# Optimization experiments

Hardware: AMD Instinct MI355X
Metric: run time of the kernel (lower is better)

## Reference

```python
import jax, jax.numpy as jnp
import numpy as np

K = 20        # kNN neighborhood size (args.k)
EPS = 1e-5    # BatchNorm eps
SLOPE = 0.2   # LeakyReLU negative slope
B, N = 8, 2048


def lrelu(x):
    return jnp.where(x >= 0, x, SLOPE * x)


def bn_cn(x):  # BatchNorm1d over [B, C, N] (training-mode batch stats, gamma=1, beta=0)
    m = jnp.mean(x, axis=(0, 2), keepdims=True)
    v = jnp.var(x, axis=(0, 2), keepdims=True)
    return (x - m) * jax.lax.rsqrt(v + EPS)


def bn_f(x):  # BatchNorm1d over [B, F]
    m = jnp.mean(x, axis=0, keepdims=True)
    v = jnp.var(x, axis=0, keepdims=True)
    return (x - m) * jax.lax.rsqrt(v + EPS)


def conv_bn(x, w):  # 1x1 Conv1d (no bias) + BN + LeakyReLU; x [B,C,N], w [O,C]
    return lrelu(bn_cn(jnp.einsum('oc,bcn->bon', w, x)))


def knn_idx(x, k):  # x [B,C,N] -> [B,N,k] nearest neighbors, self excluded
    sq = jnp.sum(x * x, axis=1)                                   # [B,N]
    pd = 2.0 * jnp.einsum('bcn,bcm->bnm', x, x) - sq[:, :, None] - sq[:, None, :]
    return jax.lax.top_k(pd, k + 1)[1][:, :, 1:]                  # drop self (max = 0)


def self_att(x, wq, wk, wv, wc):  # SelfAttention block (n_heads=1, scale_dot)
    idx = knn_idx(x, K)                                           # [B,N,K]
    feats = jnp.swapaxes(x, 1, 2)                                 # [B,N,C]
    nb = jax.vmap(lambda f, i: f[i])(feats, idx)                  # [B,N,K,C] gather
    E = wq.shape[0]
    q = feats @ wq.T                                              # [B,N,E]
    kk = nb @ wk.T                                                # [B,N,K,E]
    v = (nb - feats[:, :, None, :]) @ wv.T                        # [B,N,K,V]
    scores = jax.nn.softmax(jnp.einsum('bne,bnke->bnk', q, kk) / np.float32(np.sqrt(E)), axis=-1)
    out = jnp.einsum('bnk,bnkv->bnv', scores, v)                  # [B,N,V]
    res = conv_bn(jnp.swapaxes(out, 1, 2), wc)                    # [B,O,N]
    return jnp.concatenate([res, x], axis=1)


def setup_inputs() -> dict:
    key = jax.random.key(0)
    ks = jax.random.split(key, 32)
    w = lambda k, o, i: jax.random.normal(k, (o, i), jnp.float32) / np.float32(np.sqrt(i))
    d = {'x': jax.random.normal(ks[0], (B, 3, N), jnp.float32)}
    dims = {1: 3, 2: 64, 3: 64, 4: 128}
    j = 1
    for s, c in dims.items():
        for nm in ('wq', 'wk', 'wv', 'wc'):
            d[f'sa{s}_{nm}'] = w(ks[j], c, c); j += 1
    d['conv1_w'] = w(ks[17], 64, 6)
    d['conv2_w'] = w(ks[18], 64, 128)
    d['conv3_w'] = w(ks[19], 128, 128)
    d['conv4_w'] = w(ks[20], 256, 256)
    d['conv5_w'] = w(ks[21], 1024, 512)
    d['lin1_w'] = w(ks[22], 512, 2048); d['lin1_b'] = jnp.zeros((512,), jnp.float32)
    d['lin2_w'] = w(ks[23], 256, 512);  d['lin2_b'] = jnp.zeros((256,), jnp.float32)
    d['lin3_w'] = w(ks[24], 40, 256);   d['lin3_b'] = jnp.zeros((40,), jnp.float32)
    return d


def reference(x, sa1_wq, sa1_wk, sa1_wv, sa1_wc, sa2_wq, sa2_wk, sa2_wv, sa2_wc,
              sa3_wq, sa3_wk, sa3_wv, sa3_wc, sa4_wq, sa4_wk, sa4_wv, sa4_wc,
              conv1_w, conv2_w, conv3_w, conv4_w, conv5_w,
              lin1_w, lin1_b, lin2_w, lin2_b, lin3_w, lin3_b):
    h = self_att(x, sa1_wq, sa1_wk, sa1_wv, sa1_wc)        # [B,6,N]
    x1 = conv_bn(h, conv1_w)                               # [B,64,N]
    h = self_att(x1, sa2_wq, sa2_wk, sa2_wv, sa2_wc)       # [B,128,N]
    x2 = conv_bn(h, conv2_w)                               # [B,64,N]
    h = self_att(x2, sa3_wq, sa3_wk, sa3_wv, sa3_wc)       # [B,128,N]
    x3 = conv_bn(h, conv3_w)                               # [B,128,N]
    h = self_att(x3, sa4_wq, sa4_wk, sa4_wv, sa4_wc)       # [B,256,N]
    x4 = conv_bn(h, conv4_w)                               # [B,256,N]
    xc = jnp.concatenate([x1, x2, x3, x4], axis=1)         # [B,512,N]
    x5 = conv_bn(xc, conv5_w)                              # [B,1024,N]
    p = jnp.concatenate([jnp.max(x5, axis=2), jnp.mean(x5, axis=2)], axis=1)  # [B,2048]
    h = lrelu(bn_f(p @ lin1_w.T + lin1_b))                 # dropout = identity (eval)
    h = lrelu(bn_f(h @ lin2_w.T + lin2_b))
    return h @ lin3_w.T + lin3_b                           # [B,40]
```

## Files before the change

kernel.cpp:

```cpp
#include <hip/hip_runtime.h>
#include <math.h>

#define BB 8
#define NN 2048
#define KNB 20

typedef __attribute__((ext_vector_type(8))) short bf16x8;
typedef __attribute__((ext_vector_type(8))) _Float16 f16x8;
typedef __attribute__((ext_vector_type(4))) float f32x4;

__device__ inline unsigned short f2bf(float f) {
  union { float f; unsigned u; } v; v.f = f;
  unsigned r = v.u + 0x7FFF + ((v.u >> 16) & 1);
  return (unsigned short)(r >> 16);
}

__device__ inline float lrelu(float v) { return v >= 0.f ? v : 0.2f * v; }

template <bool F16SPLIT, bool BF16>
__global__ __launch_bounds__(256) void xprep_kernel(
    const float* __restrict__ in, int inBS, int C,
    float* __restrict__ xT, _Float16* __restrict__ hi, _Float16* __restrict__ lo,
    unsigned short* __restrict__ bf, float* __restrict__ sq) {
  __shared__ float tile[32][33];
// ... 5 lines not shown
  int tx = threadIdx.x & 31, ty = threadIdx.x >> 5;
  float s = 0.f;
  for (int yy = ty; yy < 32; yy += 8) {
    int r = r0 + yy;
    float v = (r < C) ? ip[(size_t)r * NN + c0 + tx] : 0.f;
    tile[yy][tx] = v;
    s += v * v;
  }
  ps[ty][tx] = s;
  __syncthreads();
  if (ty == 0) {
    float a = ps[0][tx];
#pragma unroll
    for (int u = 1; u < 8; ++u) a += ps[u][tx];
    atomicAdd(&sq[b * NN + c0 + tx], a);
  }
  for (int yy = ty; yy < 32; yy += 8) {
    int c = c0 + yy, r = r0 + tx;
    if (r < C) {
      float v = tile[tx][yy];
      size_t o = (size_t)b * NN * C + (size_t)c * C + r;
      xT[o] = v;
      if (F16SPLIT) {
        _Float16 hv = (_Float16)v;
        hi[o] = hv;
        lo[o] = (_Float16)(v - (float)hv);
      }
      if (BF16) bf[o] = f2bf(v);
    }
  }
}

__global__ __launch_bounds__(256) void xprep3_kernel(const float* __restrict__ in,
                                                     float* __restrict__ xT,
                                                     float* __restrict__ xs4) {
  int b = blockIdx.z;
  int n = blockIdx.x * 256 + threadIdx.x;
  const float* ip = in + (size_t)b * 3 * NN;
  float x0 = ip[n], x1 = ip[NN + n], x2 = ip[2 * NN + n];
  float s = x0 * x0 + x1 * x1 + x2 * x2;
  size_t o = (size_t)b * NN + n;
  xT[o * 3 + 0] = x0; xT[o * 3 + 1] = x1; xT[o * 3 + 2] = x2;
  *(float4*)&xs4[o * 4] = make_float4(x0, x1, x2, s);
}

__device__ inline void mw_task(const float* __restrict__ wq, const float* __restrict__ wk,
                               const float* __restrict__ wv, const float* __restrict__ wc,
                               int C, float* __restrict__ M, float* __restrict__ WCV,
                               unsigned short* __restrict__ Mb, unsigned short* __restrict__ wcvb,
                               bool emitBF, int w, int lane) {
  int total = 2 * C * C;
  if (w >= total) return;
  float a = 0.f;
  if (w < C * C) {
    int c = w / C, cp = w - c * C;
    for (int e = lane; e < C; e += 64) a += wk[e * C + c] * wq[e * C + cp];
  } else {
    int t = w - C * C;
    int o = t / C, c = t - o * C;
    for (int e = lane; e < C; e += 64) a += wc[o * C + e] * wv[e * C + c];
  }
#pragma unroll
  for (int s = 32; s > 0; s >>= 1) a += __shfl_down(a, s);
  if (lane == 0) {
    if (w < C * C) {
      M[w] = a;
      if (emitBF) Mb[w] = f2bf(a);
    } else {
      int t = w - C * C;
      WCV[t] = a;
      if (emitBF) wcvb[t] = f2bf(a);
    }
  }
}

// ... 11 lines not shown
  int wv_ = threadIdx.x >> 6;
  if (bx < 5) {
    mw_task(wq1, wk1, wv1, wc1, 3, M1, W1, nullptr, nullptr, false, bx * 4 + wv_, lane);
    return;
  }
  bx -= 5;
  if (bx < 2048) {
    mw_task(wq2, wk2, wv2, wc2, 64, M2, W2, nullptr, nullptr, false, bx * 4 + wv_, lane);
    return;
  }
  bx -= 2048;
  if (bx < 2048) {
    mw_task(wq3, wk3, wv3, wc3, 64, M3, W3, nullptr, nullptr, false, bx * 4 + wv_, lane);
    return;
  }
  bx -= 2048;
  if (bx < 8192) {
    mw_task(wq4, wk4, wv4, wc4, 128, M4, W4, Mb4, wcvb4, true, bx * 4 + wv_, lane);
    return;
  }
  bx -= 8192;
  if (bx < 256) {
    int i = bx * 256 + threadIdx.x;
    w4b[i] = f2bf(conv4_w[i]);
    return;
  }
  bx -= 256;
  {
    int i = bx * 256 + threadIdx.x;
    w5b[i] = f2bf(conv5_w[i]);
  }
}

__global__ __launch_bounds__(256) void transpose_kernel(const float* __restrict__ in, int inBS,
                                                        int R, int Cl, float* __restrict__ out) {
  __shared__ float tile[32][33];
  int b = blockIdx.z;
  const float* ip = in + (size_t)b * inBS;
  float* op = out + (size_t)b * R * Cl;
  int c0 = blockIdx.x * 32, r0 = blockIdx.y * 32;
  int tx = threadIdx.x & 31, ty = threadIdx.x >> 5;
  for (int yy = ty; yy < 32; yy += 8) {
    int r = r0 + yy, c = c0 + tx;
    tile[yy][tx] = (r < R && c < Cl) ? ip[(size_t)r * Cl + c] : 0.f;
  }
  __syncthreads();
  for (int yy = ty; yy < 32; yy += 8) {
    int c = c0 + yy, r = r0 + tx;
    if (c < Cl && r < R) op[(size_t)c * R + r] = tile[tx][yy];
  }
}

__global__ __launch_bounds__(256) void transpose_bf16_kernel(const float* __restrict__ in, int inBS,
                                                             int R, int Cl,
                                                             unsigned short* __restrict__ out) {
  __shared__ float tile[32][33];
  int b = blockIdx.z;
  const float* ip = in + (size_t)b * inBS;
  unsigned short* op = out + (size_t)b * R * Cl;
  int c0 = blockIdx.x * 32, r0 = blockIdx.y * 32;
  int tx = threadIdx.x & 31, ty = threadIdx.x >> 5;
  for (int yy = ty; yy < 32; yy += 8) {
    int r = r0 + yy, c = c0 + tx;
    tile[yy][tx] = (r < R && c < Cl) ? ip[(size_t)r * Cl + c] : 0.f;
  }
  __syncthreads();
  for (int yy = ty; yy < 32; yy += 8) {
    int c = c0 + yy, r = r0 + tx;
    if (c < Cl && r < R) op[(size_t)c * R + r] = f2bf(tile[tx][yy]);
  }
}

template <bool TOUT, bool STATS>
__global__ __launch_bounds__(256, 2) void mfma_gemm_lds_kernel(
    const unsigned short* __restrict__ A, const unsigned short* __restrict__ B,
    float* __restrict__ Z, int O, int K, float* __restrict__ gstats) {
  const int b = blockIdx.z;
  const int n0 = blockIdx.x * 128, o0 = blockIdx.y * 128;
  const int tid = threadIdx.x;
  const int wave = tid >> 6, lane = tid & 63;
  const int wo = wave >> 1, wn = wave & 1;
  const int l16 = lane & 15, q = lane >> 4;
  __shared__ unsigned short Al[2][4096];
  __shared__ unsigned short Bl[2][4096];
  const unsigned short* Ab = A + (size_t)o0 * K;
  const unsigned short* Bb = B + ((size_t)b * NN + n0) * K;

  const int p0 = tid, p1 = tid + 256;
  const int r0 = ((p0 >> 6) << 4) | (p0 & 15), c0 = ((p0 >> 4) & 3) * 8;
  const int r1 = ((p1 >> 6) << 4) | (p1 & 15), c1 = ((p1 >> 4) & 3) * 8;

  bf16x8 ar0, ar1, br0, br1;
  auto gload = [&](int k0) {
    ar0 = *(const bf16x8*)(Ab + (size_t)r0 * K + k0 + c0);
    ar1 = *(const bf16x8*)(Ab + (size_t)r1 * K + k0 + c1);
    br0 = *(const bf16x8*)(Bb + (size_t)r0 * K + k0 + c0);
    br1 = *(const bf16x8*)(Bb + (size_t)r1 * K + k0 + c1);
  };
  auto sstore = [&](int buf) {
    *(bf16x8*)&Al[buf][p0 * 8] = ar0;
    *(bf16x8*)&Al[buf][p1 * 8] = ar1;
    *(bf16x8*)&Bl[buf][p0 * 8] = br0;
    *(bf16x8*)&Bl[buf][p1 * 8] = br1;
  };

  f32x4 acc[4][4];
#pragma unroll
  for (int s = 0; s < 4; ++s)
#pragma unroll
    for (int t = 0; t < 4; ++t) acc[s][t] = (f32x4){0.f, 0.f, 0.f, 0.f};

  gload(0);
  sstore(0);
  int cur = 0;
  for (int k0 = 0; k0 < K; k0 += 32) {
    bool more = (k0 + 32) < K;
    if (more) gload(k0 + 32);
    __syncthreads();
    bf16x8 af[4], bfr[4];
#pragma unroll
    for (int s = 0; s < 4; ++s)
      af[s] = *(const bf16x8*)&Al[cur][((wo * 4 + s) * 64 + q * 16 + l16) * 8];
#pragma unroll
    for (int t = 0; t < 4; ++t)
      bfr[t] = *(const bf16x8*)&Bl[cur][((wn * 4 + t) * 64 + q * 16 + l16) * 8];
#pragma unroll
    for (int s = 0; s < 4; ++s)
#pragma unroll
      for (int t = 0; t < 4; ++t)
        acc[s][t] = __builtin_amdgcn_mfma_f32_16x16x32_bf16(af[s], bfr[t], acc[s][t], 0, 0, 0);
    if (more) sstore(cur ^ 1);
    cur ^= 1;
  }
#pragma unroll
  for (int s = 0; s < 4; ++s)
#pragma unroll
    for (int t = 0; t < 4; ++t) {
      if (TOUT) {
        int n = n0 + wn * 64 + t * 16 + l16;
        int ob = o0 + wo * 64 + s * 16 + q * 4;
        *(f32x4*)&Z[((size_t)b * NN + n) * O + ob] = acc[s][t];
      } else {
        float* zp = Z + ((size_t)b * O + o0 + wo * 64 + s * 16 + q * 4) * NN
                    + n0 + wn * 64 + t * 16 + l16;
#pragma unroll
        for (int r = 0; r < 4; ++r) zp[(size_t)r * NN] = acc[s][t][r];
      }
    }
  if (STATS) {
    float psum[16], psq[16];
#pragma unroll
    for (int s = 0; s < 4; ++s)
#pragma unroll
      for (int r = 0; r < 4; ++r) {
        float a = 0.f, sa = 0.f;
#pragma unroll
        for (int t = 0; t < 4; ++t) { float v = acc[s][t][r]; a += v; sa += v * v; }
        psum[s * 4 + r] = a; psq[s * 4 + r] = sa;
      }
#pragma unroll
    for (int i = 0; i < 16; ++i) {
#pragma unroll
      for (int mm = 1; mm < 16; mm <<= 1) {
        psum[i] += __shfl_xor(psum[i], mm);
        psq[i] += __shfl_xor(psq[i], mm);
      }
    }
    __syncthreads();
    float* sb = (float*)&Al[0][0];
    sb[tid] = 0.f;
    __syncthreads();
    if (l16 == 0) {
#pragma unroll
      for (int i = 0; i < 16; ++i) {
        int ch = wo * 64 + (i >> 2) * 16 + q * 4 + (i & 3);
        atomicAdd(&sb[ch * 2], psum[i]);
        atomicAdd(&sb[ch * 2 + 1], psq[i]);
      }
    }
    __syncthreads();
    atomicAdd(&gstats[o0 * 2 + tid], sb[tid]);
  }
}

__global__ __launch_bounds__(256, 2) void pd_mfma_sym_kernel(
    const _Float16* __restrict__ xhi, const _Float16* __restrict__ xlo, int C,
    const float* __restrict__ sq, float* __restrict__ P, int b_base) {
  const int bl = blockIdx.y;
  const int b = b_base + bl;
  int ti = 0, xx = blockIdx.x;
  while (xx >= 16 - ti) { xx -= 16 - ti; ++ti; }
  const int tj = ti + xx;
  const int n0 = ti * 128, m0 = tj * 128;
  const int tid = threadIdx.x;
  const int wave = tid >> 6, lane = tid & 63;
  const int wn_ = wave >> 1, wm_ = wave & 1;
  const int l16 = lane & 15, q = lane >> 4;
  __shared__ _Float16 Ah[4096], Al[4096], Bh[4096], Bl[4096];
  const _Float16* Ahg = xhi + ((size_t)b * NN + n0) * C;
  const _Float16* Alg = xlo + ((size_t)b * NN + n0) * C;
  const _Float16* Bhg = xhi + ((size_t)b * NN + m0) * C;
  const _Float16* Blg = xlo + ((size_t)b * NN + m0) * C;

  const int p0 = tid, p1 = tid + 256;
  const int r0 = ((p0 >> 6) << 4) | (p0 & 15), c0 = ((p0 >> 4) & 3) * 8;
  const int r1 = ((p1 >> 6) << 4) | (p1 & 15), c1 = ((p1 >> 4) & 3) * 8;

  f32x4 acc[4][4];
#pragma unroll
  for (int s = 0; s < 4; ++s)
#pragma unroll
    for (int t = 0; t < 4; ++t) acc[s][t] = (f32x4){0.f, 0.f, 0.f, 0.f};

  for (int k0 = 0; k0 < C; k0 += 32) {
    __syncthreads();
    *(f16x8*)&Ah[p0 * 8] = *(const f16x8*)(Ahg + (size_t)r0 * C + k0 + c0);
    *(f16x8*)&Ah[p1 * 8] = *(const f16x8*)(Ahg + (size_t)r1 * C + k0 + c1);
    *(f16x8*)&Al[p0 * 8] = *(const f16x8*)(Alg + (size_t)r0 * C + k0 + c0);
    *(f16x8*)&Al[p1 * 8] = *(const f16x8*)(Alg + (size_t)r1 * C + k0 + c1);
    *(f16x8*)&Bh[p0 * 8] = *(const f16x8*)(Bhg + (size_t)r0 * C + k0 + c0);
    *(f16x8*)&Bh[p1 * 8] = *(const f16x8*)(Bhg + (size_t)r1 * C + k0 + c1);
    *(f16x8*)&Bl[p0 * 8] = *(const f16x8*)(Blg + (size_t)r0 * C + k0 + c0);
    *(f16x8*)&Bl[p1 * 8] = *(const f16x8*)(Blg + (size_t)r1 * C + k0 + c1);
    __syncthreads();
    f16x8 ah[4], al[4], bh[4], blv[4];
#pragma unroll
    for (int s = 0; s < 4; ++s) {
      int pi = ((wn_ * 4 + s) * 64 + q * 16 + l16) * 8;
      ah[s] = *(const f16x8*)&Ah[pi];
      al[s] = *(const f16x8*)&Al[pi];
    }
#pragma unroll
    for (int t = 0; t < 4; ++t) {
      int pi = ((wm_ * 4 + t) * 64 + q * 16 + l16) * 8;
      bh[t] = *(const f16x8*)&Bh[pi];
      blv[t] = *(const f16x8*)&Bl[pi];
    }
#pragma unroll
    for (int s = 0; s < 4; ++s)
#pragma unroll
      for (int t = 0; t < 4; ++t) {
        acc[s][t] = __builtin_amdgcn_mfma_f32_16x16x32_f16(ah[s], bh[t], acc[s][t], 0, 0, 0);
        acc[s][t] = __builtin_amdgcn_mfma_f32_16x16x32_f16(ah[s], blv[t], acc[s][t], 0, 0, 0);
        acc[s][t] = __builtin_amdgcn_mfma_f32_16x16x32_f16(al[s], bh[t], acc[s][t], 0, 0, 0);
      }
  }
#pragma unroll
  for (int s = 0; s < 4; ++s)
#pragma unroll
    for (int t = 0; t < 4; ++t) {
      int col = m0 + wm_ * 64 + t * 16 + l16;
      float sqv = sq[b * NN + col];
      float* pp = P + ((size_t)bl * NN + n0 + wn_ * 64 + s * 16 + q * 4) * NN + col;
#pragma unroll
      for (int r = 0; r < 4; ++r) pp[(size_t)r * NN] = 2.f * acc[s][t][r] - sqv;
    }
  if (ti != tj) {
#pragma unroll
    for (int s = 0; s < 4; ++s) {
      int nb = n0 + wn_ * 64 + s * 16 + q * 4;
      float4 sqn = *(const float4*)&sq[b * NN + nb];
#pragma unroll
      for (int t = 0; t < 4; ++t) {
        int m = m0 + wm_ * 64 + t * 16 + l16;
        f32x4 ov;
        ov[0] = 2.f * acc[s][t][0] - sqn.x;
        ov[1] = 2.f * acc[s][t][1] - sqn.y;
        ov[2] = 2.f * acc[s][t][2] - sqn.z;
        ov[3] = 2.f * acc[s][t][3] - sqn.w;
        *(f32x4*)&P[((size_t)bl * NN + m) * NN + nb] = ov;
      }
    }
  }
}

__global__ __launch_bounds__(256) void topk_bsort_kernel(const float* __restrict__ P,
                                                         int* __restrict__ idx_out, int b_base) {
  const int wave = threadIdx.x >> 6;
// ... 75 lines not shown
#pragma unroll
    for (int j = k >> 1; j > 0; j >>= 1) {
#pragma unroll
      for (int i = 0; i < 32; ++i) {
        int l = i ^ j;
        if (l > i) {
          unsigned ka = key[i], kb = key[l];
          unsigned mx = ka > kb ? ka : kb;
          unsigned mn = ka > kb ? kb : ka;
          if ((i & k) == 0) { key[i] = mx; key[l] = mn; }
          else              { key[i] = mn; key[l] = mx; }
        }
      }
    }
  }
  int* op = idx_out + (size_t)(b * NN + n) * KNB;
  for (int k = 0; k < KNB; ++k) {
    unsigned best = key[0];
#pragma unroll
    for (int s = 32; s > 0; s >>= 1) {
      unsigned o = (unsigned)__shfl_xor((int)best, s);
      best = best > o ? best : o;
    }
    unsigned long long bal = __ballot(key[0] == best);
    if (lane == (int)__ffsll(bal) - 1) {
      unsigned sl = key[0] & 31u;
      op[k] = (int)(sl * 64u + (unsigned)lane);
#pragma unroll
      for (int j = 0; j < 20; ++j) key[j] = key[j + 1];
    }
  }
}

template <bool BT, bool TOUT>
__global__ __launch_bounds__(256, 2) void conv_gemm_kernel(
    const float* __restrict__ in, int inBS, int C, int O,
    const float* __restrict__ w, float* __restrict__ z) {
  const int b = blockIdx.z;
  const int n0 = blockIdx.x * 64, o0 = blockIdx.y * 64;
  const int tid = threadIdx.x;
  const int tm = tid & 15, tn = tid >> 4;
  __shared__ float Ws[16][68];
  __shared__ float Xs[16][64];
  const float* ib = in + (size_t)b * inBS;
  float acc[4][4];
#pragma unroll
  for (int i = 0; i < 4; ++i)
#pragma unroll
    for (int j = 0; j < 4; ++j) acc[i][j] = 0.f;

  for (int k0 = 0; k0 < C; k0 += 16) {
    __syncthreads();
#pragma unroll
    for (int it = 0; it < 4; ++it) {
      int i = it * 256 + tid;
      if (BT) {
        int kc = i & 15, nl = i >> 4;
        Xs[kc][nl] = ((k0 + kc) < C) ? ib[(size_t)(n0 + nl) * C + k0 + kc] : 0.f;
      } else {
        int kc = i >> 6, nl = i & 63;
        Xs[kc][nl] = ((k0 + kc) < C) ? ib[(size_t)(k0 + kc) * NN + n0 + nl] : 0.f;
      }
      int ol = i >> 4, kc2 = i & 15;
      Ws[kc2][ol] = ((o0 + ol) < O && (k0 + kc2) < C) ? w[(size_t)(o0 + ol) * C + k0 + kc2] : 0.f;
    }
    __syncthreads();
// ... 140 lines not shown
    p[k] = a;
  }
#pragma unroll
  for (int k = 0; k < KNB; ++k) {
#pragma unroll
    for (int s = 32; s > 0; s >>= 1) p[k] += __shfl_xor(p[k], s);
  }
  const float scale = (C == 128) ? 0.088388347648318447f : 0.125f;
  float mx = p[0];
#pragma unroll
  for (int k = 1; k < KNB; ++k) mx = fmaxf(mx, p[k]);
  float sum = 0.f;
#pragma unroll
  for (int k = 0; k < KNB; ++k) {
    p[k] = expf((p[k] - mx) * scale);
    sum += p[k];
  }
  float inv = 1.f / sum;
  float a0 = 0.f, a1 = 0.f;
#pragma unroll
  for (int k = 0; k < KNB; ++k) {
    a0 += p[k] * v0[k];
    if (C == 128) a1 += p[k] * v1[k];
  }
  float r0 = a0 * inv - xTb[(size_t)n * C + lane];
  float r1;
  if (C == 128) r1 = a1 * inv - xTb[(size_t)n * C + 64 + lane];
  if (BF16OUT) {
    AGGtb[(size_t)gid * C + lane] = f2bf(r0);
    if (C == 128) AGGtb[(size_t)gid * C + 64 + lane] = f2bf(r1);
  } else {
    AGGt[(size_t)gid * C + lane] = r0;
    if (C == 128) AGGt[(size_t)gid * C + 64 + lane] = r1;
  }
}

template <int C, bool BF16OUT>
__global__ __launch_bounds__(64) void att_wave_kernel(
    const float* __restrict__ xT, const float* __restrict__ UT,
    const int* __restrict__ idx, float* __restrict__ AGGt,
    unsigned short* __restrict__ AGGtb) {
  const int n = blockIdx.x & (NN - 1);
  const int b = blockIdx.x >> 11;
  const int lane = threadIdx.x;
  constexpr int CP = C + 1;
  __shared__ float nb[KNB][CP];
  __shared__ float sl[KNB];
  __shared__ int nidx[KNB];
  __shared__ float ul[C];
  const float* xTb = xT + (size_t)b * NN * C;
  if (lane < KNB) nidx[lane] = idx[(size_t)(b * NN + n) * KNB + lane] & (NN - 1);
  for (int c = lane; c < C; c += 64) ul[c] = UT[((size_t)b * NN + n) * C + c];
  __syncthreads();
  for (int i = lane; i < KNB * C; i += 64) {
    int k = i / C, c = i - k * C;
    nb[k][c] = xTb[(size_t)nidx[k] * C + c];
  }
  __syncthreads();
  float sv = -INFINITY;
  if (lane < KNB) {
    float a = 0.f;
#pragma unroll
    for (int c = 0; c < C; ++c) a += nb[lane][c] * ul[c];
    sv = a / sqrtf((float)C);
  }
  float mx = sv;
#pragma unroll
  for (int s = 32; s > 0; s >>= 1) mx = fmaxf(mx, __shfl_xor(mx, s));
  float e = (lane < KNB) ? expf(sv - mx) : 0.f;
  float sum = e;
#pragma unroll
  for (int s = 32; s > 0; s >>= 1) sum += __shfl_xor(sum, s);
  if (lane < KNB) sl[lane] = e / sum;
  __syncthreads();
  const float* xTn = xTb + (size_t)n * C;
  for (int c = lane; c < C; c += 64) {
    float a = 0.f;
#pragma unroll
    for (int k = 0; k < KNB; ++k) a += sl[k] * nb[k][c];
    float r = a - xTn[c];
    if (BF16OUT)
      AGGtb[((size_t)b * NN + n) * C + c] = f2bf(r);
    else
      AGGt[((size_t)b * NN + n) * C + c] = r;
  }
}

template <bool PRE>
__global__ __launch_bounds__(256) void bn_fused_kernel(const float* __restrict__ z, int O,
                                                       float* __restrict__ out, int outBS, int c0,
                                                       const float* __restrict__ gs) {
  int o = blockIdx.x;
  int tid = threadIdx.x;
  float m, r;
  if (PRE) {
    float s = gs[o * 2], s2 = gs[o * 2 + 1];
    m = s / (BB * NN);
    float var = s2 / (BB * NN) - m * m;
    r = rsqrtf(var + 1e-5f);
  } else {
    __shared__ float s1[256], s2[256];
    __shared__ float smv, srv;
    float a1 = 0.f, a2 = 0.f;
    for (int i = tid; i < BB * 512; i += 256) {
      int b = i >> 9, n4 = i & 511;
      float4 v = *(const float4*)&z[((size_t)b * O + o) * NN + n4 * 4];
      a1 += v.x + v.y + v.z + v.w;
      a2 += v.x * v.x + v.y * v.y + v.z * v.z + v.w * v.w;
    }
    s1[tid] = a1; s2[tid] = a2;
    __syncthreads();
    for (int st = 128; st > 0; st >>= 1) {
      if (tid < st) { s1[tid] += s1[tid + st]; s2[tid] += s2[tid + st]; }
      __syncthreads();
    }
    if (tid == 0) {
      float mm = s1[0] / (BB * NN);
// ... 158 lines not shown
}

template <int C, bool MFMA>
static inline void run_sa(const float* xin, int xbs,
                          float* xT, float* UT, float* AGGt, float* z, float* h,
                          float* sq, int* idx,
                          const float* M, const float* WCV,
                          const unsigned short* Mb, const unsigned short* wcvb,
                          unsigned short* xTb, unsigned short* AGGtb,
                          _Float16* xhi, _Float16* xlo,
                          float* D, int nbatch, hipStream_t st) {
  static_assert(C % 32 == 0, "run_sa requires C % 32 == 0");
  xprep_kernel<true, MFMA><<<dim3(NN / 32, C / 32, BB), 256, 0, st>>>(
      xin, xbs, C, xT, xhi, xlo, xTb, sq);
  for (int bb = 0; bb < BB; bb += nbatch) {
    int nbc = (BB - bb) < nbatch ? (BB - bb) : nbatch;
    pd_mfma_sym_kernel<<<dim3(136, nbc), 256, 0, st>>>(xhi, xlo, C, sq, D, bb);
    topk_bsort_kernel<<<dim3(NN / 4, nbc), 256, 0, st>>>(D, idx, bb);
  }
  if (MFMA) {
    mfma_gemm_lds_kernel<true, false><<<dim3(NN / 128, C / 128, BB), 256, 0, st>>>(
        (const unsigned short*)Mb, xTb, UT, C, C, nullptr);
    att_wave_reg_kernel<C, true><<<BB * NN / 4, 256, 0, st>>>(xT, UT, idx, nullptr, AGGtb);
    mfma_gemm_lds_kernel<false, false><<<dim3(NN / 128, C / 128, BB), 256, 0, st>>>(
        (const unsigned short*)wcvb, AGGtb, z, C, C, nullptr);
  } else {
    conv_gemm_kernel<false, true><<<dim3(NN / 64, C / 64, BB), 256, 0, st>>>(xin, xbs, C, C, M, UT);
    att_wave_reg_kernel<C, false><<<BB * NN / 4, 256, 0, st>>>(xT, UT, idx, AGGt, nullptr);
    conv_gemm_kernel<true, false><<<dim3(NN / 64, C / 64, BB), 256, 0, st>>>(AGGt, NN * C, C, C, WCV, z);
  }
  bn_copy_kernel<<<2 * C, 256, 0, st>>>(z, C, xin, xbs, h);
}

static inline void run_sa3(const float* xin,
                           float* xT, float* U, float* UT, float* AGGt, float* AGG,
                           float* z, float* h, float* xs4, int* idx,
                           const float* M, const float* WCV, hipStream_t st) {
  xprep3_kernel<<<dim3(NN / 256, 1, BB), 256, 0, st>>>(xin, xT, xs4);
  topk_c3_kernel<<<dim3(NN / 4, BB), 256, 0, st>>>(xs4, idx);
  conv_gemm_kernel<false, false><<<dim3(NN / 64, 1, BB), 256, 0, st>>>(xin, 3 * NN, 3, 3, M, U);
  transpose_kernel<<<dim3(NN / 32, 1, BB), 256, 0, st>>>(U, 3 * NN, 3, NN, UT);
  att_wave_kernel<3, false><<<BB * NN, 64, 0, st>>>(xT, UT, idx, AGGt, nullptr);
  transpose_kernel<<<dim3(1, NN / 32, BB), 256, 0, st>>>(AGGt, NN * 3, NN, 3, AGG);
  conv_gemm_kernel<false, false><<<dim3(NN / 64, 1, BB), 256, 0, st>>>(AGG, 3 * NN, 3, 3, WCV, z);
  bn_copy_kernel<<<6, 256, 0, st>>>(z, 3, xin, 3 * NN, h);
}

static inline void run_conv_bn(const float* in, int inBS, int Cin, int O, const float* w,
                               float* z, float* out, int outBS, int c0, hipStream_t st) {
  run_conv(in, inBS, Cin, O, w, z, st);
  bn_fused_kernel<false><<<O, 256, 0, st>>>(z, O, out, outBS, c0, nullptr);
}

extern "C" void kernel_launch(void* const* d_in, const int* in_sizes, int n_in,
                              void* d_out, int out_size, void* d_ws, size_t ws_size,
                              hipStream_t stream) {
  const float* x = (const float*)d_in[0];
  SAW sa1{(const float*)d_in[1], (const float*)d_in[2], (const float*)d_in[3], (const float*)d_in[4]};
  SAW sa2{(const float*)d_in[5], (const float*)d_in[6], (const float*)d_in[7], (const float*)d_in[8]};
  SAW sa3{(const float*)d_in[9], (const float*)d_in[10], (const float*)d_in[11], (const float*)d_in[12]};
  SAW sa4{(const float*)d_in[13], (const float*)d_in[14], (const float*)d_in[15], (const float*)d_in[16]};
  const float* conv1_w = (const float*)d_in[17];
  const float* conv2_w = (const float*)d_in[18];
  const float* conv3_w = (const float*)d_in[19];
  const float* conv4_w = (const float*)d_in[20];
  const float* conv5_w = (const float*)d_in[21];
  const float* lin1_w = (const float*)d_in[22];
  const float* lin1_b = (const float*)d_in[23];
  const float* lin2_w = (const float*)d_in[24];
  const float* lin2_b = (const float*)d_in[25];
  const float* lin3_w = (const float*)d_in[26];
  const float* lin3_b = (const float*)d_in[27];

  char* ws = (char*)d_ws;
  size_t off = 0;
  auto take = [&](size_t bytes) -> void* {
    void* p = ws + off;
    off += (bytes + 255) & ~(size_t)255;
    return p;
  };
  float* sqR  = (float*)take((size_t)3 * BB * NN * 4);
  float* statsR = (float*)take((size_t)(256 + 1024) * 2 * 4);
  float* xs4  = (float*)take((size_t)BB * NN * 4 * 4);
  int*   idx  = (int*)take((size_t)BB * NN * KNB * 4);
  float* Mall = (float*)take((size_t)4 * 128 * 128 * 4);
  float* Wall = (float*)take((size_t)4 * 128 * 128 * 4);
  unsigned short* Mb4   = (unsigned short*)take((size_t)128 * 128 * 2);
  unsigned short* wcvb4 = (unsigned short*)take((size_t)128 * 128 * 2);
  unsigned short* w4b  = (unsigned short*)take((size_t)256 * 256 * 2);
  unsigned short* w5b  = (unsigned short*)take((size_t)1024 * 512 * 2);
  float* U    = (float*)take((size_t)BB * 128 * NN * 4);
  float* AGG  = (float*)take((size_t)BB * 128 * NN * 4);
  float* h    = (float*)take((size_t)BB * 256 * NN * 4);
  float* z    = (float*)take((size_t)BB * 1024 * NN * 4);
  float* xc   = (float*)take((size_t)BB * 512 * NN * 4);
  float* p    = (float*)take((size_t)BB * 2048 * 4);
  float* t1   = (float*)take((size_t)BB * 512 * 4);
  float* t2   = (float*)take((size_t)BB * 256 * 4);
  (void)n_in; (void)in_sizes; (void)out_size;

  float* M1 = Mall + 0 * 16384; float* W1 = Wall + 0 * 16384;
  float* M2 = Mall + 1 * 16384; float* W2 = Wall + 1 * 16384;
  float* M3 = Mall + 2 * 16384; float* W3 = Wall + 2 * 16384;
  float* M4 = Mall + 3 * 16384; float* W4 = Wall + 3 * 16384;
  float* stats4 = statsR;
  float* stats5 = statsR + 256 * 2;

  float* xT = AGG;
  float* AGGt64 = AGG + (size_t)BB * NN * 64;
  float* UT = h;
  float* AGGt1 = z;
  unsigned short* xTb   = (unsigned short*)((char*)h + (size_t)BB * 128 * NN * 4);
  unsigned short* AGGtb = (unsigned short*)((char*)z + (size_t)16 * 1024 * 1024);
  unsigned short* hTb   = (unsigned short*)U;
  unsigned short* xcTb  = (unsigned short*)U;
  _Float16* xhi = (_Float16*)h;
  _Float16* xlo = (_Float16*)((char*)h + (size_t)BB * NN * 128 * 2);

  size_t dfull = (size_t)BB * NN * NN * 4;
  bool fullD = (ws_size > off + dfull + 4096);
  float* D = fullD ? (float*)take(dfull) : z;
  int nbatch = fullD ? BB : 4;

  hipMemsetAsync(sqR, 0, (size_t)3 * BB * NN * 4 + (size_t)(256 + 1024) * 2 * 4, stream);
  weight_prep_kernel<<<5 + 2048 + 2048 + 8192 + 256 + 2048, 256, 0, stream>>>(
      sa1.wq, sa1.wk, sa1.wv, sa1.wc, sa2.wq, sa2.wk, sa2.wv, sa2.wc,
      sa3.wq, sa3.wk, sa3.wv, sa3.wc, sa4.wq, sa4.wk, sa4.wv, sa4.wc,
      conv4_w, conv5_w, M1, W1, M2, W2, M3, W3, M4, W4, Mb4, wcvb4, w4b, w5b);

  run_sa3(x, xT, U, UT, AGGt1, AGG, z, h, xs4, idx, M1, W1, stream);
  run_conv_bn(h, 6 * NN, 6, 64, conv1_w, z, xc, 512 * NN, 0, stream);
  run_sa<64, false>(xc + 0 * NN, 512 * NN, xT, UT, AGGt64, z, h,
                    sqR + 0 * BB * NN, idx, M2, W2, nullptr, nullptr, xTb, AGGtb, xhi, xlo,
                    D, nbatch, stream);
  run_conv_bn(h, 128 * NN, 128, 64, conv2_w, z, xc, 512 * NN, 64, stream);
  run_sa<64, false>(xc + 64 * NN, 512 * NN, xT, UT, AGGt64, z, h,
                    sqR + 1 * BB * NN, idx, M3, W3, nullptr, nullptr, xTb, AGGtb, xhi, xlo,
                    D, nbatch, stream);
  run_conv_bn(h, 128 * NN, 128, 128, conv3_w, z, xc, 512 * NN, 128, stream);
  run_sa<128, true>(xc + 128 * NN, 512 * NN, xT, UT, nullptr, z, h,
                    sqR + 2 * BB * NN, idx, M4, W4, Mb4, wcvb4, xTb, AGGtb, xhi, xlo,
                    D, nbatch, stream);
  transpose_bf16_kernel<<<dim3(NN / 32, 8, BB), 256, 0, stream>>>(h, 256 * NN, 256, NN, hTb);
  mfma_gemm_lds_kernel<false, true><<<dim3(NN / 128, 2, BB), 256, 0, stream>>>(
      w4b, hTb, z, 256, 256, stats4);
  bn_fused_kernel<true><<<256, 256, 0, stream>>>(z, 256, xc, 512 * NN, 256, stats4);
  transpose_bf16_kernel<<<dim3(NN / 32, 16, BB), 256, 0, stream>>>(xc, 512 * NN, 512, NN, xcTb);
  mfma_gemm_lds_kernel<false, true><<<dim3(NN / 128, 8, BB), 256, 0, stream>>>(
      w5b, xcTb, z, 1024, 512, stats5);
  bn_pool_kernel<true><<<1024, 256, 0, stream>>>(z, p, stats5);
  linear_kernel<<<BB * 512, 64, 0, stream>>>(p, 2048, 512, lin1_w, lin1_b, t1);
  bnf_kernel<<<2, 256, 0, stream>>>(t1, 512);
  linear_kernel<<<BB * 256, 64, 0, stream>>>(t1, 512, 256, lin2_w, lin2_b, t2);
  bnf_kernel<<<1, 256, 0, stream>>>(t2, 256);
  linear_kernel<<<BB * 40, 64, 0, stream>>>(t2, 256, 40, lin3_w, lin3_b, (float*)d_out);
}
```

Measured before the change: 850.4 us.

## Load GEMM and pairwise-distance tiles directly into LDS with async double buffering

Both MFMA GEMM kernels now use global_load_lds to copy operand tiles straight from global memory into shared memory, with no round trip through registers. The pairwise-distance kernel gains double-buffered LDS, so the next K-slice loads while the current one is consumed, and it needs one barrier per iteration instead of two. The dense GEMM's launch bound is raised to allow three blocks per CU, which relies on the registers freed by dropping the staging values. Correctness now depends on the compiler placing the right vmcnt waits before the barrier for the asynchronous LDS writes, and the pd kernel's doubled LDS use may lower its occupancy.

```diff
diff --git a/kernel.cpp b/kernel.cpp
--- a/kernel.cpp
+++ b/kernel.cpp
@@ -187,7 +187,7 @@
 }
 
 template <bool TOUT, bool STATS>
-__global__ __launch_bounds__(256, 2) void mfma_gemm_lds_kernel(
+__global__ __launch_bounds__(256, 3) void mfma_gemm_lds_kernel(
     const unsigned short* __restrict__ A, const unsigned short* __restrict__ B,
     float* __restrict__ Z, int O, int K, float* __restrict__ gstats) {
   const int b = blockIdx.z;
@@ -205,19 +205,16 @@
   const int r0 = ((p0 >> 6) << 4) | (p0 & 15), c0 = ((p0 >> 4) & 3) * 8;
   const int r1 = ((p1 >> 6) << 4) | (p1 & 15), c1 = ((p1 >> 4) & 3) * 8;
 
-  bf16x8 ar0, ar1, br0, br1;
-  auto gload = [&](int k0) {
-    ar0 = *(const bf16x8*)(Ab + (size_t)r0 * K + k0 + c0);
-    ar1 = *(const bf16x8*)(Ab + (size_t)r1 * K + k0 + c1);
-    br0 = *(const bf16x8*)(Bb + (size_t)r0 * K + k0 + c0);
-    br1 = *(const bf16x8*)(Bb + (size_t)r1 * K + k0 + c1);
+  auto glds = [&](int buf, int k0) {
+    __builtin_amdgcn_global_load_lds((const unsigned int*)(Ab + (size_t)r0 * K + k0 + c0),
+                                     (unsigned int*)&Al[buf][p0 * 8], 16, 0, 0);
+    __builtin_amdgcn_global_load_lds((const unsigned int*)(Ab + (size_t)r1 * K + k0 + c1),
+                                     (unsigned int*)&Al[buf][p1 * 8], 16, 0, 0);
+    __builtin_amdgcn_global_load_lds((const unsigned int*)(Bb + (size_t)r0 * K + k0 + c0),
+                                     (unsigned int*)&Bl[buf][p0 * 8], 16, 0, 0);
+    __builtin_amdgcn_global_load_lds((const unsigned int*)(Bb + (size_t)r1 * K + k0 + c1),
+                                     (unsigned int*)&Bl[buf][p1 * 8], 16, 0, 0);
   };
-  auto sstore = [&](int buf) {
-    *(bf16x8*)&Al[buf][p0 * 8] = ar0;
-    *(bf16x8*)&Al[buf][p1 * 8] = ar1;
-    *(bf16x8*)&Bl[buf][p0 * 8] = br0;
-    *(bf16x8*)&Bl[buf][p1 * 8] = br1;
-  };
 
   f32x4 acc[4][4];
 #pragma unroll
@@ -225,13 +222,11 @@
 #pragma unroll
     for (int t = 0; t < 4; ++t) acc[s][t] = (f32x4){0.f, 0.f, 0.f, 0.f};
 
-  gload(0);
-  sstore(0);
+  glds(0, 0);
   int cur = 0;
   for (int k0 = 0; k0 < K; k0 += 32) {
-    bool more = (k0 + 32) < K;
-    if (more) gload(k0 + 32);
-    __syncthreads();
+    __syncthreads();
+    if (k0 + 32 < K) glds(cur ^ 1, k0 + 32);
     bf16x8 af[4], bfr[4];
 #pragma unroll
     for (int s = 0; s < 4; ++s)
@@ -244,7 +239,6 @@
 #pragma unroll
       for (int t = 0; t < 4; ++t)
         acc[s][t] = __builtin_amdgcn_mfma_f32_16x16x32_bf16(af[s], bfr[t], acc[s][t], 0, 0, 0);
-    if (more) sstore(cur ^ 1);
     cur ^= 1;
   }
 #pragma unroll
@@ -311,7 +305,7 @@
   const int wave = tid >> 6, lane = tid & 63;
   const int wn_ = wave >> 1, wm_ = wave & 1;
   const int l16 = lane & 15, q = lane >> 4;
-  __shared__ _Float16 Ah[4096], Al[4096], Bh[4096], Bl[4096];
+  __shared__ _Float16 Ah[2][4096], Alo[2][4096], Bh[2][4096], Blo[2][4096];
   const _Float16* Ahg = xhi + ((size_t)b * NN + n0) * C;
   const _Float16* Alg = xlo + ((size_t)b * NN + n0) * C;
   const _Float16* Bhg = xhi + ((size_t)b * NN + m0) * C;
@@ -321,35 +315,48 @@
   const int r0 = ((p0 >> 6) << 4) | (p0 & 15), c0 = ((p0 >> 4) & 3) * 8;
   const int r1 = ((p1 >> 6) << 4) | (p1 & 15), c1 = ((p1 >> 4) & 3) * 8;
 
+  auto glds = [&](int buf, int k0) {
+    __builtin_amdgcn_global_load_lds((const unsigned int*)(Ahg + (size_t)r0 * C + k0 + c0),
+                                     (unsigned int*)&Ah[buf][p0 * 8], 16, 0, 0);
+    __builtin_amdgcn_global_load_lds((const unsigned int*)(Ahg + (size_t)r1 * C + k0 + c1),
+                                     (unsigned int*)&Ah[buf][p1 * 8], 16, 0, 0);
+    __builtin_amdgcn_global_load_lds((const unsigned int*)(Alg + (size_t)r0 * C + k0 + c0),
+                                     (unsigned int*)&Alo[buf][p0 * 8], 16, 0, 0);
+    __builtin_amdgcn_global_load_lds((const unsigned int*)(Alg + (size_t)r1 * C + k0 + c1),
+                                     (unsigned int*)&Alo[buf][p1 * 8], 16, 0, 0);
+    __builtin_amdgcn_global_load_lds((const unsigned int*)(Bhg + (size_t)r0 * C + k0 + c0),
+                                     (unsigned int*)&Bh[buf][p0 * 8], 16, 0, 0);
+    __builtin_amdgcn_global_load_lds((const unsigned int*)(Bhg + (size_t)r1 * C + k0 + c1),
+                                     (unsigned int*)&Bh[buf][p1 * 8], 16, 0, 0);
+    __builtin_amdgcn_global_load_lds((const unsigned int*)(Blg + (size_t)r0 * C + k0 + c0),
+                                     (unsigned int*)&Blo[buf][p0 * 8], 16, 0, 0);
+    __builtin_amdgcn_global_load_lds((const unsigned int*)(Blg + (size_t)r1 * C + k0 + c1),
+                                     (unsigned int*)&Blo[buf][p1 * 8], 16, 0, 0);
+  };
+
   f32x4 acc[4][4];
 #pragma unroll
   for (int s = 0; s < 4; ++s)
 #pragma unroll
     for (int t = 0; t < 4; ++t) acc[s][t] = (f32x4){0.f, 0.f, 0.f, 0.f};
 
+  glds(0, 0);
+  int cur = 0;
   for (int k0 = 0; k0 < C; k0 += 32) {
     __syncthreads();
-    *(f16x8*)&Ah[p0 * 8] = *(const f16x8*)(Ahg + (size_t)r0 * C + k0 + c0);
-    *(f16x8*)&Ah[p1 * 8] = *(const f16x8*)(Ahg + (size_t)r1 * C + k0 + c1);
-    *(f16x8*)&Al[p0 * 8] = *(const f16x8*)(Alg + (size_t)r0 * C + k0 + c0);
-    *(f16x8*)&Al[p1 * 8] = *(const f16x8*)(Alg + (size_t)r1 * C + k0 + c1);
-    *(f16x8*)&Bh[p0 * 8] = *(const f16x8*)(Bhg + (size_t)r0 * C + k0 + c0);
-    *(f16x8*)&Bh[p1 * 8] = *(const f16x8*)(Bhg + (size_t)r1 * C + k0 + c1);
-    *(f16x8*)&Bl[p0 * 8] = *(const f16x8*)(Blg + (size_t)r0 * C + k0 + c0);
-    *(f16x8*)&Bl[p1 * 8] = *(const f16x8*)(Blg + (size_t)r1 * C + k0 + c1);
-    __syncthreads();
+    if (k0 + 32 < C) glds(cur ^ 1, k0 + 32);
     f16x8 ah[4], al[4], bh[4], blv[4];
 #pragma unroll
     for (int s = 0; s < 4; ++s) {
       int pi = ((wn_ * 4 + s) * 64 + q * 16 + l16) * 8;
-      ah[s] = *(const f16x8*)&Ah[pi];
-      al[s] = *(const f16x8*)&Al[pi];
+      ah[s] = *(const f16x8*)&Ah[cur][pi];
+      al[s] = *(const f16x8*)&Alo[cur][pi];
     }
 #pragma unroll
     for (int t = 0; t < 4; ++t) {
       int pi = ((wm_ * 4 + t) * 64 + q * 16 + l16) * 8;
-      bh[t] = *(const f16x8*)&Bh[pi];
-      blv[t] = *(const f16x8*)&Bl[pi];
+      bh[t] = *(const f16x8*)&Bh[cur][pi];
+      blv[t] = *(const f16x8*)&Blo[cur][pi];
     }
 #pragma unroll
     for (int s = 0; s < 4; ++s)
@@ -359,6 +366,7 @@
         acc[s][t] = __builtin_amdgcn_mfma_f32_16x16x32_f16(ah[s], blv[t], acc[s][t], 0, 0, 0);
         acc[s][t] = __builtin_amdgcn_mfma_f32_16x16x32_f16(al[s], bh[t], acc[s][t], 0, 0, 0);
       }
+    cur ^= 1;
   }
 #pragma unroll
   for (int s = 0; s < 4; ++s)
```

Result: no change. 866.6 us (+1.9%).

## Fuse first self-attention block into one kernel and widen conv5 GEMM tile

Applied to the files above, without the earlier changes.

Replaces the first self-attention stage's chain of small GEMM, transpose, per-point attention-wave and second GEMM launches with a single per-point kernel. Each thread computes the query projection, 20-neighbour scores, softmax, aggregation and output projection in registers, reading the packed xs4 buffer. It also adds a bf16 MFMA GEMM with a 128x256 output tile per block for the conv5 layer, meant to get more reuse per LDS load. The larger accumulator array raises register pressure and may reduce occupancy.

```diff
diff --git a/kernel.cpp b/kernel.cpp
--- a/kernel.cpp
+++ b/kernel.cpp
@@ -61,7 +61,6 @@
 }
 
 __global__ __launch_bounds__(256) void xprep3_kernel(const float* __restrict__ in,
-                                                     float* __restrict__ xT,
                                                      float* __restrict__ xs4) {
   int b = blockIdx.z;
   int n = blockIdx.x * 256 + threadIdx.x;
@@ -69,7 +68,6 @@
   float x0 = ip[n], x1 = ip[NN + n], x2 = ip[2 * NN + n];
   float s = x0 * x0 + x1 * x1 + x2 * x2;
   size_t o = (size_t)b * NN + n;
-  xT[o * 3 + 0] = x0; xT[o * 3 + 1] = x1; xT[o * 3 + 2] = x2;
   *(float4*)&xs4[o * 4] = make_float4(x0, x1, x2, s);
 }
 
@@ -147,25 +145,6 @@
   }
 }
 
-__global__ __launch_bounds__(256) void transpose_kernel(const float* __restrict__ in, int inBS,
-                                                        int R, int Cl, float* __restrict__ out) {
-  __shared__ float tile[32][33];
-  int b = blockIdx.z;
-  const float* ip = in + (size_t)b * inBS;
-  float* op = out + (size_t)b * R * Cl;
-  int c0 = blockIdx.x * 32, r0 = blockIdx.y * 32;
-  int tx = threadIdx.x & 31, ty = threadIdx.x >> 5;
-  for (int yy = ty; yy < 32; yy += 8) {
-    int r = r0 + yy, c = c0 + tx;
-    tile[yy][tx] = (r < R && c < Cl) ? ip[(size_t)r * Cl + c] : 0.f;
-  }
-  __syncthreads();
-  for (int yy = ty; yy < 32; yy += 8) {
-    int c = c0 + yy, r = r0 + tx;
-    if (c < Cl && r < R) op[(size_t)c * R + r] = tile[tx][yy];
-  }
-}
-
 __global__ __launch_bounds__(256) void transpose_bf16_kernel(const float* __restrict__ in, int inBS,
                                                              int R, int Cl,
                                                              unsigned short* __restrict__ out) {
@@ -271,6 +250,115 @@
         float a = 0.f, sa = 0.f;
 #pragma unroll
         for (int t = 0; t < 4; ++t) { float v = acc[s][t][r]; a += v; sa += v * v; }
+        psum[s * 4 + r] = a; psq[s * 4 + r] = sa;
+      }
+#pragma unroll
+    for (int i = 0; i < 16; ++i) {
+#pragma unroll
+      for (int mm = 1; mm < 16; mm <<= 1) {
+        psum[i] += __shfl_xor(psum[i], mm);
+        psq[i] += __shfl_xor(psq[i], mm);
+      }
+    }
+    __syncthreads();
+    float* sb = (float*)&Al[0][0];
+    sb[tid] = 0.f;
+    __syncthreads();
+    if (l16 == 0) {
+#pragma unroll
+      for (int i = 0; i < 16; ++i) {
+        int ch = wo * 64 + (i >> 2) * 16 + q * 4 + (i & 3);
+        atomicAdd(&sb[ch * 2], psum[i]);
+        atomicAdd(&sb[ch * 2 + 1], psq[i]);
+      }
+    }
+    __syncthreads();
+    atomicAdd(&gstats[o0 * 2 + tid], sb[tid]);
+  }
+}
+
+__global__ __launch_bounds__(256, 2) void mfma_gemm_n256_kernel(
+    const unsigned short* __restrict__ A, const unsigned short* __restrict__ B,
+    float* __restrict__ Z, int O, int K, float* __restrict__ gstats) {
+  const int b = blockIdx.z;
+  const int n0 = blockIdx.x * 256, o0 = blockIdx.y * 128;
+  const int tid = threadIdx.x;
+  const int wave = tid >> 6, lane = tid & 63;
+  const int wo = wave >> 1, wn = wave & 1;
+  const int l16 = lane & 15, q = lane >> 4;
+  __shared__ unsigned short Al[2][4096];
+  __shared__ unsigned short Bl[2][8192];
+  const unsigned short* Ab = A + (size_t)o0 * K;
+  const unsigned short* Bb = B + ((size_t)b * NN + n0) * K;
+
+  const int pA0 = tid, pA1 = tid + 256;
+  const int rA0 = ((pA0 >> 6) << 4) | (pA0 & 15), cA0 = ((pA0 >> 4) & 3) * 8;
+  const int rA1 = ((pA1 >> 6) << 4) | (pA1 & 15), cA1 = ((pA1 >> 4) & 3) * 8;
+
+  bf16x8 ar0, ar1, br[4];
+  auto gload = [&](int k0) {
+    ar0 = *(const bf16x8*)(Ab + (size_t)rA0 * K + k0 + cA0);
+    ar1 = *(const bf16x8*)(Ab + (size_t)rA1 * K + k0 + cA1);
+#pragma unroll
+    for (int i = 0; i < 4; ++i) {
+      int p = tid + 256 * i;
+      int r = ((p >> 6) << 4) | (p & 15), c = ((p >> 4) & 3) * 8;
+      br[i] = *(const bf16x8*)(Bb + (size_t)r * K + k0 + c);
+    }
+  };
+  auto sstore = [&](int buf) {
+    *(bf16x8*)&Al[buf][pA0 * 8] = ar0;
+    *(bf16x8*)&Al[buf][pA1 * 8] = ar1;
+#pragma unroll
+    for (int i = 0; i < 4; ++i) *(bf16x8*)&Bl[buf][(tid + 256 * i) * 8] = br[i];
+  };
+
+  f32x4 acc[4][8];
+#pragma unroll
+  for (int s = 0; s < 4; ++s)
+#pragma unroll
+    for (int t = 0; t < 8; ++t) acc[s][t] = (f32x4){0.f, 0.f, 0.f, 0.f};
+
+  gload(0);
+  sstore(0);
+  int cur = 0;
+  for (int k0 = 0; k0 < K; k0 += 32) {
+    bool more = (k0 + 32) < K;
+    if (more) gload(k0 + 32);
+    __syncthreads();
+    bf16x8 af[4], bfr[8];
+#pragma unroll
+    for (int s = 0; s < 4; ++s)
+      af[s] = *(const bf16x8*)&Al[cur][((wo * 4 + s) * 64 + q * 16 + l16) * 8];
+#pragma unroll
+    for (int t = 0; t < 8; ++t)
+      bfr[t] = *(const bf16x8*)&Bl[cur][((wn * 8 + t) * 64 + q * 16 + l16) * 8];
+#pragma unroll
+    for (int s = 0; s < 4; ++s)
+#pragma unroll
+      for (int t = 0; t < 8; ++t)
+        acc[s][t] = __builtin_amdgcn_mfma_f32_16x16x32_bf16(af[s], bfr[t], acc[s][t], 0, 0, 0);
+    if (more) sstore(cur ^ 1);
+    cur ^= 1;
+  }
+#pragma unroll
+  for (int s = 0; s < 4; ++s)
+#pragma unroll
+    for (int t = 0; t < 8; ++t) {
+      float* zp = Z + ((size_t)b * O + o0 + wo * 64 + s * 16 + q * 4) * NN
+                  + n0 + wn * 128 + t * 16 + l16;
+#pragma unroll
+      for (int r = 0; r < 4; ++r) zp[(size_t)r * NN] = acc[s][t][r];
+    }
+  {
+    float psum[16], psq[16];
+#pragma unroll
+    for (int s = 0; s < 4; ++s)
+#pragma unroll
+      for (int r = 0; r < 4; ++r) {
+        float a = 0.f, sa = 0.f;
+#pragma unroll
+        for (int t = 0; t < 8; ++t) { float v = acc[s][t][r]; a += v; sa += v * v; }
         psum[s * 4 + r] = a; psq[s * 4 + r] = sa;
       }
 #pragma unroll
@@ -500,6 +588,49 @@
   }
 }
 
+__global__ __launch_bounds__(256) void sa1_fused_kernel(
+    const float* __restrict__ xs4, const int* __restrict__ idx,
+    const float* __restrict__ M, const float* __restrict__ W,
+    float* __restrict__ z) {
+  __shared__ float Ms[9], Ws9[9];
+  int t = threadIdx.x;
+  if (t < 9) Ms[t] = M[t];
+  else if (t < 18) Ws9[t - 9] = W[t - 9];
+  __syncthreads();
+  int gid = blockIdx.x * 256 + t;
+  int b = gid >> 11, n = gid & (NN - 1);
+  const float4* xp = (const float4*)(xs4 + (size_t)b * NN * 4);
+  float4 me = xp[n];
+  float u0 = Ms[0] * me.x + Ms[1] * me.y + Ms[2] * me.z;
+  float u1 = Ms[3] * me.x + Ms[4] * me.y + Ms[5] * me.z;
+  float u2 = Ms[6] * me.x + Ms[7] * me.y + Ms[8] * me.z;
+  const float scale = 0.57735026919f;
+  const int* ip = idx + (size_t)gid * KNB;
+  float nbx[KNB], nby[KNB], nbz[KNB], sc[KNB];
+#pragma unroll
+  for (int k = 0; k < KNB; ++k) {
+    int m = ip[k] & (NN - 1);
+    float4 c = xp[m];
+    nbx[k] = c.x; nby[k] = c.y; nbz[k] = c.z;
+    sc[k] = (c.x * u0 + c.y * u1 + c.z * u2) * scale;
+  }
+  float mx = sc[0];
+#pragma unroll
+  for (int k = 1; k < KNB; ++k) mx = fmaxf(mx, sc[k]);
+  float sum = 0.f;
+#pragma unroll
+  for (int k = 0; k < KNB; ++k) { sc[k] = expf(sc[k] - mx); sum += sc[k]; }
+  float inv = 1.f / sum;
+  float a0 = 0.f, a1 = 0.f, a2 = 0.f;
+#pragma unroll
+  for (int k = 0; k < KNB; ++k) { a0 += sc[k] * nbx[k]; a1 += sc[k] * nby[k]; a2 += sc[k] * nbz[k]; }
+  a0 = a0 * inv - me.x; a1 = a1 * inv - me.y; a2 = a2 * inv - me.z;
+  float* zb = z + (size_t)b * 3 * NN;
+  zb[n]          = Ws9[0] * a0 + Ws9[1] * a1 + Ws9[2] * a2;
+  zb[NN + n]     = Ws9[3] * a0 + Ws9[4] * a1 + Ws9[5] * a2;
+  zb[2 * NN + n] = Ws9[6] * a0 + Ws9[7] * a1 + Ws9[8] * a2;
+}
+
 template <bool BT, bool TOUT>
 __global__ __launch_bounds__(256, 2) void conv_gemm_kernel(
     const float* __restrict__ in, int inBS, int C, int O,
@@ -706,57 +837,6 @@
   } else {
     AGGt[(size_t)gid * C + lane] = r0;
     if (C == 128) AGGt[(size_t)gid * C + 64 + lane] = r1;
-  }
-}
-
-template <int C, bool BF16OUT>
-__global__ __launch_bounds__(64) void att_wave_kernel(
-    const float* __restrict__ xT, const float* __restrict__ UT,
-    const int* __restrict__ idx, float* __restrict__ AGGt,
-    unsigned short* __restrict__ AGGtb) {
-  const int n = blockIdx.x & (NN - 1);
-  const int b = blockIdx.x >> 11;
-  const int lane = threadIdx.x;
-  constexpr int CP = C + 1;
-  __shared__ float nb[KNB][CP];
-  __shared__ float sl[KNB];
-  __shared__ int nidx[KNB];
-  __shared__ float ul[C];
-  const float* xTb = xT + (size_t)b * NN * C;
-  if (lane < KNB) nidx[lane] = idx[(size_t)(b * NN + n) * KNB + lane] & (NN - 1);
-  for (int c = lane; c < C; c += 64) ul[c] = UT[((size_t)b * NN + n) * C + c];
-  __syncthreads();
-  for (int i = lane; i < KNB * C; i += 64) {
-    int k = i / C, c = i - k * C;
-    nb[k][c] = xTb[(size_t)nidx[k] * C + c];
-  }
-  __syncthreads();
-  float sv = -INFINITY;
-  if (lane < KNB) {
-    float a = 0.f;
-#pragma unroll
-    for (int c = 0; c < C; ++c) a += nb[lane][c] * ul[c];
-    sv = a / sqrtf((float)C);
-  }
-  float mx = sv;
-#pragma unroll
-  for (int s = 32; s > 0; s >>= 1) mx = fmaxf(mx, __shfl_xor(mx, s));
-  float e = (lane < KNB) ? expf(sv - mx) : 0.f;
-  float sum = e;
-#pragma unroll
-  for (int s = 32; s > 0; s >>= 1) sum += __shfl_xor(sum, s);
-  if (lane < KNB) sl[lane] = e / sum;
-  __syncthreads();
-  const float* xTn = xTb + (size_t)n * C;
-  for (int c = lane; c < C; c += 64) {
-    float a = 0.f;
-#pragma unroll
-    for (int k = 0; k < KNB; ++k) a += sl[k] * nb[k][c];
-    float r = a - xTn[c];
-    if (BF16OUT)
-      AGGtb[((size_t)b * NN + n) * C + c] = f2bf(r);
-    else
-      AGGt[((size_t)b * NN + n) * C + c] = r;
   }
 }
 
@@ -981,17 +1061,11 @@
   bn_copy_kernel<<<2 * C, 256, 0, st>>>(z, C, xin, xbs, h);
 }
 
-static inline void run_sa3(const float* xin,
-                           float* xT, float* U, float* UT, float* AGGt, float* AGG,
-                           float* z, float* h, float* xs4, int* idx,
+static inline void run_sa3(const float* xin, float* z, float* h, float* xs4, int* idx,
                            const float* M, const float* WCV, hipStream_t st) {
-  xprep3_kernel<<<dim3(NN / 256, 1, BB), 256, 0, st>>>(xin, xT, xs4);
+  xprep3_kernel<<<dim3(NN / 256, 1, BB), 256, 0, st>>>(xin, xs4);
   topk_c3_kernel<<<dim3(NN / 4, BB), 256, 0, st>>>(xs4, idx);
-  conv_gemm_kernel<false, false><<<dim3(NN / 64, 1, BB), 256, 0, st>>>(xin, 3 * NN, 3, 3, M, U);
-  transpose_kernel<<<dim3(NN / 32, 1, BB), 256, 0, st>>>(U, 3 * NN, 3, NN, UT);
-  att_wave_kernel<3, false><<<BB * NN, 64, 0, st>>>(xT, UT, idx, AGGt, nullptr);
-  transpose_kernel<<<dim3(1, NN / 32, BB), 256, 0, st>>>(AGGt, NN * 3, NN, 3, AGG);
-  conv_gemm_kernel<false, false><<<dim3(NN / 64, 1, BB), 256, 0, st>>>(AGG, 3 * NN, 3, 3, WCV, z);
+  sa1_fused_kernel<<<BB * NN / 256, 256, 0, st>>>(xs4, idx, M, WCV, z);
   bn_copy_kernel<<<6, 256, 0, st>>>(z, 3, xin, 3 * NN, h);
 }
 
@@ -1058,7 +1132,6 @@
   float* xT = AGG;
   float* AGGt64 = AGG + (size_t)BB * NN * 64;
   float* UT = h;
-  float* AGGt1 = z;
   unsigned short* xTb   = (unsigned short*)((char*)h + (size_t)BB * 128 * NN * 4);
   unsigned short* AGGtb = (unsigned short*)((char*)z + (size_t)16 * 1024 * 1024);
   unsigned short* hTb   = (unsigned short*)U;
@@ -1077,7 +1150,7 @@
       sa3.wq, sa3.wk, sa3.wv, sa3.wc, sa4.wq, sa4.wk, sa4.wv, sa4.wc,
       conv4_w, conv5_w, M1, W1, M2, W2, M3, W3, M4, W4, Mb4, wcvb4, w4b, w5b);
 
-  run_sa3(x, xT, U, UT, AGGt1, AGG, z, h, xs4, idx, M1, W1, stream);
+  run_sa3(x, z, h, xs4, idx, M1, W1, stream);
   run_conv_bn(h, 6 * NN, 6, 64, conv1_w, z, xc, 512 * NN, 0, stream);
   run_sa<64, false>(xc + 0 * NN, 512 * NN, xT, UT, AGGt64, z, h,
                     sqR + 0 * BB * NN, idx, M2, W2, nullptr, nullptr, xTb, AGGtb, xhi, xlo,
@@ -1095,7 +1168,7 @@
       w4b, hTb, z, 256, 256, stats4);
   bn_fused_kernel<true><<<256, 256, 0, stream>>>(z, 256, xc, 512 * NN, 256, stats4);
   transpose_bf16_kernel<<<dim3(NN / 32, 16, BB), 256, 0, stream>>>(xc, 512 * NN, 512, NN, xcTb);
-  mfma_gemm_lds_kernel<false, true><<<dim3(NN / 128, 8, BB), 256, 0, stream>>>(
+  mfma_gemm_n256_kernel<<<dim3(NN / 256, 8, BB), 256, 0, stream>>>(
       w5b, xcTb, z, 1024, 512, stats5);
   bn_pool_kernel<true><<<1024, 256, 0, stream>>>(z, p, stats5);
   linear_kernel<<<BB * 512, 64, 0, stream>>>(p, 2048, 512, lin1_w, lin1_b, t1);
```

Result: faster. 828.6 us (-2.6%).
